# Performance work log

Hardware: AMD Instinct MI355X
Metric: run time of the kernel (lower is better)

The kernel has to match this reference:

```python
import jax, jax.numpy as jnp
import numpy as np

B, N, C, H = 8, 1024, 768, 12
WBITS, ABITS, PGABITS = 8, 8, 4
TH = 0.99  # greater-than mask threshold on MSB softmax


def quant(x, bits):
    """Fixed-point quantize to `bits` bits, straight-through estimator."""
    step = 2.0 ** (1 - bits)
    q = jnp.round(x / step) * step
    return x + jax.lax.stop_gradient(q - x)


def setup_inputs() -> dict:
    key = jax.random.key(0)
    k1, k2, k3 = jax.random.split(key, 3)
    x = jax.random.normal(k1, (B, N, C), jnp.float32)
    # qkv: QLinear(dim, 3*dim, bias=False); proj: QLinear(dim, dim, bias=True)
    w_qkv = jax.random.normal(k2, (3 * C, C), jnp.float32) * (C ** -0.5)
    w_proj = jax.random.normal(k3, (C, C), jnp.float32) * (C ** -0.5)
    b_proj = jnp.zeros((C,), jnp.float32)
    return {"x": x, "w_qkv": w_qkv, "w_proj": w_proj, "b_proj": b_proj}


def reference(x, w_qkv, w_proj, b_proj):
    d = C // H
    scale = d ** -0.5
    # QLinear: quantize activations and weights, then matmul (no qkv bias)
    qkv = quant(x, ABITS) @ quant(w_qkv, WBITS).T            # [B,N,3C]
    qkv = qkv.reshape(B, N, 3, H, d).transpose(2, 0, 3, 1, 4)  # [3,B,H,N,d]
    qkv = quant(qkv, ABITS)
    q, k, v = qkv[0], qkv[1], qkv[2]
    # low-precision MSB pass
    q_msb = quant(q, PGABITS)
    k_msb = quant(k, PGABITS)
    attn_msb = jax.nn.softmax(
        jnp.einsum('bhqd,bhkd->bhqk', q_msb, k_msb) * scale, axis=-1)
    # GreaterThan with straight-through backward (identity grad)
    gt = (attn_msb > TH).astype(attn_msb.dtype)
    mask = attn_msb + jax.lax.stop_gradient(gt - attn_msb)
    # full-precision pass, masked pre-softmax
    attn = jnp.einsum('bhqd,bhkd->bhqk', q, k) * scale * mask
    attn = quant(jax.nn.softmax(attn, axis=-1), ABITS)
    out = jnp.einsum('bhqk,bhkd->bhqd', attn, v)             # [B,H,N,d]
    out = out.transpose(0, 2, 1, 3).reshape(B, N, C)
    return quant(out, ABITS) @ quant(w_proj, WBITS).T + b_proj
```

## Files before the change

### kernel.cpp

```cpp
#include <hip/hip_runtime.h>

#define NB 8
#define NSEQ 1024
#define NC 768
#define NH 12
#define ND 64
#define NM 8192

typedef _Float16 v8h __attribute__((ext_vector_type(8)));
typedef float v4f __attribute__((ext_vector_type(4)));
typedef int   v4i __attribute__((ext_vector_type(4)));

__device__ __forceinline__ float q8f(float x){ return rintf(x*128.f)*0.0078125f; }
__device__ __forceinline__ int imax2(int a, int b){ return a > b ? a : b; }
__device__ __forceinline__ int imin2(int a, int b){ return a < b ? a : b; }

__device__ __forceinline__ int swz(int r, int g){ return (r<<6) + (((g ^ (r & 7)) & 7)<<3); }

__device__ __forceinline__ void async_cp16(const void* g, void* l) {
  __builtin_amdgcn_global_load_lds(
      (const __attribute__((address_space(1))) unsigned int*)g,
      (__attribute__((address_space(3))) unsigned int*)l, 16, 0, 0);
}

__device__ __forceinline__ int idot64(const int* a, const int* b) {
  int si = 0;
#if __has_builtin(__builtin_amdgcn_sdot4)
#pragma unroll
  for (int j = 0; j < 16; j++) si = __builtin_amdgcn_sdot4(a[j], b[j], si, false);
#else
  const char* ca = (const char*)a;
  const char* cb = (const char*)b;
#pragma unroll
  for (int j = 0; j < 64; j++) si += (int)ca[j] * (int)cb[j];
#endif
  return si;
}

__global__ __launch_bounds__(256) void k_pre(const float* __restrict__ x,
                                             const float* __restrict__ wq,
                                             _Float16* __restrict__ xt,
                                             _Float16* __restrict__ wqt) {
  int b = blockIdx.x;
  const float* src; _Float16* dst; int gid;
  if (b < 3072) { src = x;  dst = xt;  gid = b*256 + threadIdx.x; }
  else          { src = wq; dst = wqt; gid = (b-3072)*256 + threadIdx.x; }
  int tile = gid / 12288;
  int rem  = gid - tile*12288;
  int chunk = rem >> 10, idx = rem & 1023;
  int r = idx >> 3, g = idx & 7;
  const float* s = src + (size_t)(tile*128 + r)*768 + chunk*64 + g*8;
  float4 v0 = *(const float4*)s, v1 = *(const float4*)(s + 4);
  v8h o;
  o[0]=(_Float16)q8f(v0.x); o[1]=(_Float16)q8f(v0.y); o[2]=(_Float16)q8f(v0.z); o[3]=(_Float16)q8f(v0.w);
  o[4]=(_Float16)q8f(v1.x); o[5]=(_Float16)q8f(v1.y); o[6]=(_Float16)q8f(v1.z); o[7]=(_Float16)q8f(v1.w);
  *(v8h*)&dst[((size_t)tile*12 + chunk)*8192 + swz(r, g)] = o;
}

__global__ __launch_bounds__(512, 2) void k_qk(const _Float16* __restrict__ xt,
                                               const _Float16* __restrict__ wqt,
                                               const float* __restrict__ bias,
                                               char* __restrict__ QmI,
                                               char* __restrict__ KmI,
                                               float* __restrict__ out) {
  if (blockIdx.x >= 192) {
    int gid = (blockIdx.x - 192)*512 + threadIdx.x;
    int c4 = gid % 192;
    ((float4*)out)[gid] = ((const float4*)bias)[c4];
    return;
  }
  __shared__ _Float16 S[65536];
  _Float16* SA = S;
  _Float16* SB = S + 32768;

  const int tid  = threadIdx.x;
  const int lane = tid & 63;
  const int quad = lane >> 4;
  const int l15  = lane & 15;
  const int wid  = tid >> 6;
  const int wm   = wid >> 2;
  const int wn   = wid & 3;
  const int bx = blockIdx.x & 31, by = blockIdx.x >> 5;
  const int m0 = bx * 256, n0 = by * 256;

  const _Float16* Abase = xt  + (size_t)(2*bx) * 12 * 8192;
  const _Float16* Bbase = wqt + (size_t)(2*by) * 12 * 8192;

  auto stage_half = [&](const _Float16* src, _Float16* dst) {
#pragma unroll
    for (int s = 0; s < 2; s++) {
      int base = (wid*2 + s)*512;
      async_cp16(src + base + lane*8, dst + base);
    }
  };

  v4f acc[8][4] = {};

  stage_half(Abase,               SA);
  stage_half(Abase + 12*8192,     SA + 8192);
  stage_half(Bbase,               SB);
  stage_half(Bbase + 12*8192,     SB + 8192);
  asm volatile("s_waitcnt vmcnt(0)" ::: "memory");
  __builtin_amdgcn_s_barrier();

#pragma unroll 1
  for (int kc = 0; kc < 12; kc++) {
    const int buf = kc & 1;
    const _Float16* A  = &SA[(buf*2 + wm)*8192];
    const _Float16* Bh = &SB[(buf*2 + (wn>>1))*8192];
    _Float16* SAn = &SA[(buf^1)*16384];
    _Float16* SBn = &SB[(buf^1)*16384];

    if (kc + 1 < 12) {
      stage_half(Abase + (size_t)(kc+1)*8192,        SAn);
      stage_half(Abase + (size_t)(12 + kc+1)*8192,   SAn + 8192);
    }

    v8h bf[4][2];
#pragma unroll
    for (int nt = 0; nt < 4; nt++)
#pragma unroll
      for (int ks = 0; ks < 2; ks++)
        bf[nt][ks] = *(const v8h*)&Bh[swz((wn&1)*64 + nt*16 + l15, ks*4 + quad)];

#pragma unroll
    for (int p = 0; p < 4; p++) {
      v8h a[2][2];
#pragma unroll
      for (int mt = 0; mt < 2; mt++)
#pragma unroll
        for (int ks = 0; ks < 2; ks++)
          a[mt][ks] = *(const v8h*)&A[swz((p*2 + mt)*16 + l15, ks*4 + quad)];
      __builtin_amdgcn_s_setprio(1);
#pragma unroll
      for (int ks = 0; ks < 2; ks++)
#pragma unroll
        for (int nt = 0; nt < 4; nt++) {
          acc[p*2+0][nt] = __builtin_amdgcn_mfma_f32_16x16x32_f16(a[0][ks], bf[nt][ks], acc[p*2+0][nt], 0, 0, 0);
          acc[p*2+1][nt] = __builtin_amdgcn_mfma_f32_16x16x32_f16(a[1][ks], bf[nt][ks], acc[p*2+1][nt], 0, 0, 0);
        }
      __builtin_amdgcn_s_setprio(0);
      if (p == 0 && kc + 1 < 12) {
        stage_half(Bbase + (size_t)(kc+1)*8192,        SBn);
        stage_half(Bbase + (size_t)(12 + kc+1)*8192,   SBn + 8192);
      }
    }
    asm volatile("s_waitcnt vmcnt(0)" ::: "memory");
    __builtin_amdgcn_s_barrier();
  }

  char* P8 = (char*)S;
#pragma unroll
  for (int fr = 0; fr < 8; fr++)
#pragma unroll
    for (int nt = 0; nt < 4; nt++)
#pragma unroll
      for (int rr = 0; rr < 4; rr++) {
        float v = q8f(acc[fr][nt][rr]);
        int qi = (int)rintf(v * 8.f);
        int rl = wm*128 + fr*16 + quad*4 + rr;
        int cl = wn*64 + nt*16 + l15;
        P8[rl*272 + cl] = (char)qi;
      }
  __syncthreads();
  const int which = (by >= 3);
  int c0 = n0 - which*768;
#pragma unroll
  for (int t = 0; t < 8; t++) {
    int idx = tid + t*512;
    int r = idx >> 4, cg = idx & 15;
    v4i val = *(const v4i*)&P8[r*272 + cg*16];
    if (!which) {
      *(v4i*)&QmI[(size_t)(m0 + r)*768 + c0 + cg*16] = val;
    } else {
      int m = m0 + r, n = m & 1023, bI = m >> 10;
      int col = c0 + cg*16;
      int h = col >> 6, d0 = col & 63;
      *(v4i*)&KmI[(((size_t)(bI*NH + h)*1024 + n) << 6) + d0] = val;
    }
  }
}

__global__ __launch_bounds__(256) void k_attn(const char* __restrict__ QmI,
                                              const char* __restrict__ KmI,
                                              const float* __restrict__ x,
                                              const float* __restrict__ wqkv,
                                              const float* __restrict__ wproj,
                                              float* __restrict__ out) {
  __shared__ char  S2[2][16384];
  __shared__ float rowm[128];
  __shared__ int   cand[128];
  __shared__ int   hrowA[128];
  __shared__ int   hcolA[128];
  __shared__ float qf[64], kf[64], vf[64];
  __shared__ float od[64];
  __shared__ float pps;
  __shared__ int   cnt, hcnt;

  const int tid  = threadIdx.x;
  const int lane = tid & 63;
  const int quad = lane >> 4;
  const int l15  = lane & 15;
  const int wid  = tid >> 6;
  const int R0   = wid * 16;
  const int bh = blockIdx.x;
  const int q0 = blockIdx.y * 128;
  const int bb = bh / NH, hb = bh % NH;
  const size_t mrow = (size_t)bb * NSEQ;
  const int hoff = hb * 64;
  const char* KmB = KmI + (size_t)bh * 1024 * 64;

  if (tid == 0) { cnt = 0; hcnt = 0; }

  auto stageK = [&](int kp, int bi) {
#pragma unroll
    for (int s = 0; s < 4; s++) {
      int seg = wid*4 + s;
      async_cp16(KmB + kp*16384 + seg*1024 + lane*16, &S2[bi][seg*1024]);
    }
  };

  v4i aQ[2];
#pragma unroll
  for (int b2 = 0; b2 < 2; b2++)
    aQ[b2] = *(const v4i*)&QmI[(mrow + q0 + b2*64 + R0 + l15)*768 + hoff + quad*16];

  int lm[2][4], lm2[2][4];
#pragma unroll
  for (int b2 = 0; b2 < 2; b2++)
#pragma unroll
    for (int r = 0; r < 4; r++) { lm[b2][r] = -1073741824; lm2[b2][r] = -1073741824; }

  stageK(0, 0);
#pragma unroll 1
  for (int kp = 0; kp < 4; kp++) {
    if (kp + 1 < 4) {
      stageK(kp + 1, (kp + 1) & 1);
      asm volatile("s_waitcnt vmcnt(4)" ::: "memory");
    } else {
      asm volatile("s_waitcnt vmcnt(0)" ::: "memory");
    }
    __builtin_amdgcn_s_barrier();
#pragma unroll
    for (int g64 = 0; g64 < 4; g64++) {
      const char* Ks = &S2[kp & 1][g64*4096];
      v4i c0a[4] = {}, c1a[4] = {};
      __builtin_amdgcn_s_setprio(1);
#pragma unroll
      for (int nt = 0; nt < 4; nt++) {
        v4i b = *(const v4i*)&Ks[(nt*16 + l15)*64 + quad*16];
        c0a[nt] = __builtin_amdgcn_mfma_i32_16x16x64_i8(aQ[0], b, c0a[nt], 0, 0, 0);
        c1a[nt] = __builtin_amdgcn_mfma_i32_16x16x64_i8(aQ[1], b, c1a[nt], 0, 0, 0);
      }
      __builtin_amdgcn_s_setprio(0);
#pragma unroll
      for (int r = 0; r < 4; r++) {
        int g0 = imax2(imax2(c0a[0][r], c0a[1][r]), imax2(c0a[2][r], c0a[3][r]));
        lm2[0][r] = imax2(lm2[0][r], imin2(lm[0][r], g0));
        lm[0][r]  = imax2(lm[0][r], g0);
        int g1 = imax2(imax2(c1a[0][r], c1a[1][r]), imax2(c1a[2][r], c1a[3][r]));
        lm2[1][r] = imax2(lm2[1][r], imin2(lm[1][r], g1));
        lm[1][r]  = imax2(lm[1][r], g1);
      }
    }
    __builtin_amdgcn_s_barrier();
  }
#pragma unroll
  for (int b2 = 0; b2 < 2; b2++)
#pragma unroll
    for (int r = 0; r < 4; r++) {
      int m = lm[b2][r], m2 = lm2[b2][r];
#pragma unroll
      for (int o = 1; o < 16; o <<= 1) {
        int om  = __shfl_xor(m, o);
        int om2 = __shfl_xor(m2, o);
        m2 = imax2(imax2(m2, om2), imin2(m, om));
        m  = imax2(m, om);
      }
      if (l15 == 0 && (m - m2) > 2304) {
        int row = b2*64 + R0 + quad*4 + r;
        rowm[row] = (float)m * 0.001953125f;
        int ix = atomicAdd(&cnt, 1);
        cand[ix] = row;
      }
    }
  __syncthreads();

  int nc = cnt;
  for (int ci = wid; ci < nc; ci += 4) {
    int row = cand[ci];
    float m = rowm[row];
    const int* qrow = (const int*)&QmI[(mrow + q0 + row)*768 + hoff];
    int qw[16];
#pragma unroll
    for (int j = 0; j < 16; j++) qw[j] = qrow[j];
    float l = 0.f, bmax = -1e30f;
    int bcol = 0;
    for (int t = 0; t < 16; t++) {
      const int* kb = (const int*)&KmB[(size_t)(t*64 + lane)*64];
      int si = idot64(qw, kb);
      float s = (float)si * 0.001953125f;
      l += expf(s - m);
      if (s > bmax) { bmax = s; bcol = t*64 + lane; }
    }
#pragma unroll
    for (int o = 1; o < 64; o <<= 1) {
      l += __shfl_xor(l, o);
      float ov = __shfl_xor(bmax, o);
      int   oc = __shfl_xor(bcol, o);
      if (ov > bmax || (ov == bmax && oc < bcol)) { bmax = ov; bcol = oc; }
    }
    if (lane == 0 && (1.0f / l) > 0.99f) {
      int ix = atomicAdd(&hcnt, 1);
      hrowA[ix] = row; hcolA[ix] = bcol;
    }
  }
  __syncthreads();

  int nh = hcnt;
  for (int hi = 0; hi < nh; hi++) {
    int row = hrowA[hi], cst = hcolA[hi];
    if (tid < 192) {
      int d = tid & 63, part = tid >> 6;
      int wrow = part*768 + hoff + d;
      int xrow = (part == 0) ? (int)(mrow + q0 + row) : (int)(mrow + cst);
      const float* xr = &x[(size_t)xrow*768];
      const float* wr = &wqkv[(size_t)wrow*768];
      float s = 0.f;
      for (int k = 0; k < 768; k++) s += q8f(xr[k]) * q8f(wr[k]);
      float v = q8f(s);
      if (part == 0) qf[d] = v; else if (part == 1) kf[d] = v; else vf[d] = v;
    }
    __syncthreads();
    if (tid == 0) {
      float s = 0.f;
      for (int d = 0; d < 64; d++) s += qf[d]*kf[d];
      float sf = s * 0.125f;
      float m2 = fmaxf(sf, 0.f);
      float l2 = expf(sf - m2) + 1023.f*expf(-m2);
      pps = rintf(expf(sf - m2)/l2*128.f)*0.0078125f;
    }
    __syncthreads();
    float p = pps;
    if (p != 0.f) {
      if (tid < 64) od[tid] = q8f(p * vf[tid]);
      __syncthreads();
      for (int c = tid; c < 768; c += 256) {
        const float* wr = &wproj[(size_t)c*768 + hoff];
        float s = 0.f;
        for (int d = 0; d < 64; d++) s += od[d] * q8f(wr[d]);
        atomicAdd(&out[(mrow + q0 + row)*768 + c], s);
      }
    }
    __syncthreads();
  }
}

extern "C" void kernel_launch(void* const* d_in, const int* in_sizes, int n_in,
                              void* d_out, int out_size, void* d_ws, size_t ws_size,
                              hipStream_t stream) {
  const float* x      = (const float*)d_in[0];
  const float* w_qkv  = (const float*)d_in[1];
  const float* w_proj = (const float*)d_in[2];
  const float* b_proj = (const float*)d_in[3];
  float* out = (float*)d_out;

  char* p = (char*)d_ws;
  _Float16* xt  = (_Float16*)p;  p += (size_t)NM*768*2;
  _Float16* wqt = (_Float16*)p;  p += (size_t)1536*768*2;
  char* QmI = p;  p += (size_t)NM*768;
  char* KmI = p;  p += (size_t)NM*768;

  k_pre <<<dim3(3648), dim3(256), 0, stream>>>(x, w_qkv, xt, wqt);
  k_qk  <<<dim3(192 + 3072), dim3(512), 0, stream>>>(xt, wqt, b_proj, QmI, KmI, out);
  k_attn<<<dim3(96, 8), dim3(256), 0, stream>>>(QmI, KmI, x, w_qkv, w_proj, out);
}
```

Before: 121.4 us.

## Keep full K tile resident in swizzled LDS and reuse it for candidate rows

```diff
diff --git a/kernel.cpp b/kernel.cpp
--- a/kernel.cpp
+++ b/kernel.cpp
@@ -187,7 +187,7 @@
                                               const float* __restrict__ wqkv,
                                               const float* __restrict__ wproj,
                                               float* __restrict__ out) {
-  __shared__ char  S2[2][16384];
+  __shared__ char  S2[65536];
   __shared__ float rowm[128];
   __shared__ int   cand[128];
   __shared__ int   hrowA[128];
@@ -212,11 +212,14 @@
 
   if (tid == 0) { cnt = 0; hcnt = 0; }
 
-  auto stageK = [&](int kp, int bi) {
+  const int rl  = lane >> 2;
+  const int gsw = (lane & 3) ^ (rl & 3);
+  auto stageK = [&](int kp) {
 #pragma unroll
     for (int s = 0; s < 4; s++) {
       int seg = wid*4 + s;
-      async_cp16(KmB + kp*16384 + seg*1024 + lane*16, &S2[bi][seg*1024]);
+      async_cp16(KmB + kp*16384 + (seg*16 + rl)*64 + (gsw<<4),
+                 &S2[kp*16384 + seg*1024]);
     }
   };
 
@@ -224,6 +227,7 @@
 #pragma unroll
   for (int b2 = 0; b2 < 2; b2++)
     aQ[b2] = *(const v4i*)&QmI[(mrow + q0 + b2*64 + R0 + l15)*768 + hoff + quad*16];
+  asm volatile("s_waitcnt vmcnt(0)" ::: "memory");
 
   int lm[2][4], lm2[2][4];
 #pragma unroll
@@ -231,24 +235,22 @@
 #pragma unroll
     for (int r = 0; r < 4; r++) { lm[b2][r] = -1073741824; lm2[b2][r] = -1073741824; }
 
-  stageK(0, 0);
+  stageK(0);
+  stageK(1);
 #pragma unroll 1
   for (int kp = 0; kp < 4; kp++) {
-    if (kp + 1 < 4) {
-      stageK(kp + 1, (kp + 1) & 1);
-      asm volatile("s_waitcnt vmcnt(4)" ::: "memory");
-    } else {
-      asm volatile("s_waitcnt vmcnt(0)" ::: "memory");
-    }
+    if (kp < 3) asm volatile("s_waitcnt vmcnt(4)" ::: "memory");
+    else        asm volatile("s_waitcnt vmcnt(0)" ::: "memory");
     __builtin_amdgcn_s_barrier();
+    if (kp + 2 < 4) stageK(kp + 2);
 #pragma unroll
     for (int g64 = 0; g64 < 4; g64++) {
-      const char* Ks = &S2[kp & 1][g64*4096];
+      const char* Ks = &S2[kp*16384 + g64*4096];
       v4i c0a[4] = {}, c1a[4] = {};
       __builtin_amdgcn_s_setprio(1);
 #pragma unroll
       for (int nt = 0; nt < 4; nt++) {
-        v4i b = *(const v4i*)&Ks[(nt*16 + l15)*64 + quad*16];
+        v4i b = *(const v4i*)&Ks[(nt*16 + l15)*64 + ((quad ^ (l15 & 3))<<4)];
         c0a[nt] = __builtin_amdgcn_mfma_i32_16x16x64_i8(aQ[0], b, c0a[nt], 0, 0, 0);
         c1a[nt] = __builtin_amdgcn_mfma_i32_16x16x64_i8(aQ[1], b, c1a[nt], 0, 0, 0);
       }
@@ -263,7 +265,6 @@
         lm[1][r]  = imax2(lm[1][r], g1);
       }
     }
-    __builtin_amdgcn_s_barrier();
   }
 #pragma unroll
   for (int b2 = 0; b2 < 2; b2++)
@@ -287,6 +288,7 @@
   __syncthreads();
 
   int nc = cnt;
+  const int xr = lane & 3;
   for (int ci = wid; ci < nc; ci += 4) {
     int row = cand[ci];
     float m = rowm[row];
@@ -297,11 +299,19 @@
     float l = 0.f, bmax = -1e30f;
     int bcol = 0;
     for (int t = 0; t < 16; t++) {
-      const int* kb = (const int*)&KmB[(size_t)(t*64 + lane)*64];
-      int si = idot64(qw, kb);
+      int rk = t*64 + lane;
+      const char* kbase = &S2[rk*64];
+      int kw[16];
+#pragma unroll
+      for (int g4 = 0; g4 < 4; g4++) {
+        v4i kv = *(const v4i*)&kbase[((g4 ^ xr)<<4)];
+        kw[g4*4+0] = kv[0]; kw[g4*4+1] = kv[1];
+        kw[g4*4+2] = kv[2]; kw[g4*4+3] = kv[3];
+      }
+      int si = idot64(qw, kw);
       float s = (float)si * 0.001953125f;
       l += expf(s - m);
-      if (s > bmax) { bmax = s; bcol = t*64 + lane; }
+      if (s > bmax) { bmax = s; bcol = rk; }
     }
 #pragma unroll
     for (int o = 1; o < 64; o <<= 1) {
@@ -324,10 +334,10 @@
       int d = tid & 63, part = tid >> 6;
       int wrow = part*768 + hoff + d;
       int xrow = (part == 0) ? (int)(mrow + q0 + row) : (int)(mrow + cst);
-      const float* xr = &x[(size_t)xrow*768];
+      const float* xr2 = &x[(size_t)xrow*768];
       const float* wr = &wqkv[(size_t)wrow*768];
       float s = 0.f;
-      for (int k = 0; k < 768; k++) s += q8f(xr[k]) * q8f(wr[k]);
+      for (int k = 0; k < 768; k++) s += q8f(xr2[k]) * q8f(wr[k]);
       float v = q8f(s);
       if (part == 0) qf[d] = v; else if (part == 1) kf[d] = v; else vf[d] = v;
     }
```

Result: slower. 132.3 us (+9.0%).

## Fuse input quantization into QK GEMM, removing the pre-pass kernel

Applied to the files above, without the earlier changes.

```diff
diff --git a/kernel.cpp b/kernel.cpp
--- a/kernel.cpp
+++ b/kernel.cpp
@@ -17,48 +17,28 @@
 
 __device__ __forceinline__ int swz(int r, int g){ return (r<<6) + (((g ^ (r & 7)) & 7)<<3); }
 
+__device__ __forceinline__ int idot64(const int* a, const int* b) {
+  int si = 0;
+#if __has_builtin(__builtin_amdgcn_sdot4)
+#pragma unroll
+  for (int j = 0; j < 16; j++) si = __builtin_amdgcn_sdot4(a[j], b[j], si, false);
+#else
+  const char* ca = (const char*)a;
+  const char* cb = (const char*)b;
+#pragma unroll
+  for (int j = 0; j < 64; j++) si += (int)ca[j] * (int)cb[j];
+#endif
+  return si;
+}
+
 __device__ __forceinline__ void async_cp16(const void* g, void* l) {
   __builtin_amdgcn_global_load_lds(
       (const __attribute__((address_space(1))) unsigned int*)g,
       (__attribute__((address_space(3))) unsigned int*)l, 16, 0, 0);
 }
 
-__device__ __forceinline__ int idot64(const int* a, const int* b) {
-  int si = 0;
-#if __has_builtin(__builtin_amdgcn_sdot4)
-#pragma unroll
-  for (int j = 0; j < 16; j++) si = __builtin_amdgcn_sdot4(a[j], b[j], si, false);
-#else
-  const char* ca = (const char*)a;
-  const char* cb = (const char*)b;
-#pragma unroll
-  for (int j = 0; j < 64; j++) si += (int)ca[j] * (int)cb[j];
-#endif
-  return si;
-}
-
-__global__ __launch_bounds__(256) void k_pre(const float* __restrict__ x,
-                                             const float* __restrict__ wq,
-                                             _Float16* __restrict__ xt,
-                                             _Float16* __restrict__ wqt) {
-  int b = blockIdx.x;
-  const float* src; _Float16* dst; int gid;
-  if (b < 3072) { src = x;  dst = xt;  gid = b*256 + threadIdx.x; }
-  else          { src = wq; dst = wqt; gid = (b-3072)*256 + threadIdx.x; }
-  int tile = gid / 12288;
-  int rem  = gid - tile*12288;
-  int chunk = rem >> 10, idx = rem & 1023;
-  int r = idx >> 3, g = idx & 7;
-  const float* s = src + (size_t)(tile*128 + r)*768 + chunk*64 + g*8;
-  float4 v0 = *(const float4*)s, v1 = *(const float4*)(s + 4);
-  v8h o;
-  o[0]=(_Float16)q8f(v0.x); o[1]=(_Float16)q8f(v0.y); o[2]=(_Float16)q8f(v0.z); o[3]=(_Float16)q8f(v0.w);
-  o[4]=(_Float16)q8f(v1.x); o[5]=(_Float16)q8f(v1.y); o[6]=(_Float16)q8f(v1.z); o[7]=(_Float16)q8f(v1.w);
-  *(v8h*)&dst[((size_t)tile*12 + chunk)*8192 + swz(r, g)] = o;
-}
-
-__global__ __launch_bounds__(512, 2) void k_qk(const _Float16* __restrict__ xt,
-                                               const _Float16* __restrict__ wqt,
+__global__ __launch_bounds__(512, 2) void k_qk(const float* __restrict__ x,
+                                               const float* __restrict__ wqkv,
                                                const float* __restrict__ bias,
                                                char* __restrict__ QmI,
                                                char* __restrict__ KmI,
@@ -83,25 +63,35 @@
   const int bx = blockIdx.x & 31, by = blockIdx.x >> 5;
   const int m0 = bx * 256, n0 = by * 256;
 
-  const _Float16* Abase = xt  + (size_t)(2*bx) * 12 * 8192;
-  const _Float16* Bbase = wqt + (size_t)(2*by) * 12 * 8192;
-
-  auto stage_half = [&](const _Float16* src, _Float16* dst) {
-#pragma unroll
-    for (int s = 0; s < 2; s++) {
-      int base = (wid*2 + s)*512;
-      async_cp16(src + base + lane*8, dst + base);
-    }
+  const int h   = tid >> 8;
+  const int t2  = tid & 255;
+  const int rr_ = t2 >> 1;
+  const int gp  = (t2 & 1) * 4;
+
+  auto ldq = [&](const float* src, int row0, int kc, int g0, float4* f) {
+    const float* sp = src + (size_t)(row0 + h*128 + rr_)*768 + kc*64 + g0*8;
+    f[0] = ((const float4*)sp)[0]; f[1] = ((const float4*)sp)[1];
+    f[2] = ((const float4*)sp)[2]; f[3] = ((const float4*)sp)[3];
   };
+  auto wrq = [&](_Float16* dstbuf, int g0, const float4* f) {
+#pragma unroll
+    for (int gi = 0; gi < 2; gi++) {
+      const float* ff = (const float*)&f[gi*2];
+      v8h o;
+#pragma unroll
+      for (int j = 0; j < 8; j++) o[j] = (_Float16)q8f(ff[j]);
+      *(v8h*)&dstbuf[h*8192 + swz(rr_, g0 + gi)] = o;
+    }
+  };
 
   v4f acc[8][4] = {};
-
-  stage_half(Abase,               SA);
-  stage_half(Abase + 12*8192,     SA + 8192);
-  stage_half(Bbase,               SB);
-  stage_half(Bbase + 12*8192,     SB + 8192);
-  asm volatile("s_waitcnt vmcnt(0)" ::: "memory");
-  __builtin_amdgcn_s_barrier();
+  float4 fa[4], fb[4];
+
+  ldq(x,    m0, 0, gp,     fa);  wrq(SA, gp,     fa);
+  ldq(x,    m0, 0, gp + 2, fa);  wrq(SA, gp + 2, fa);
+  ldq(wqkv, n0, 0, gp,     fb);  wrq(SB, gp,     fb);
+  ldq(wqkv, n0, 0, gp + 2, fb);  wrq(SB, gp + 2, fb);
+  __syncthreads();
 
 #pragma unroll 1
   for (int kc = 0; kc < 12; kc++) {
@@ -110,11 +100,9 @@
     const _Float16* Bh = &SB[(buf*2 + (wn>>1))*8192];
     _Float16* SAn = &SA[(buf^1)*16384];
     _Float16* SBn = &SB[(buf^1)*16384];
-
-    if (kc + 1 < 12) {
-      stage_half(Abase + (size_t)(kc+1)*8192,        SAn);
-      stage_half(Abase + (size_t)(12 + kc+1)*8192,   SAn + 8192);
-    }
+    const bool pre = (kc + 1 < 12);
+
+    if (pre) ldq(x, m0, kc + 1, gp, fa);
 
     v8h bf[4][2];
 #pragma unroll
@@ -140,13 +128,14 @@
           acc[p*2+1][nt] = __builtin_amdgcn_mfma_f32_16x16x32_f16(a[1][ks], bf[nt][ks], acc[p*2+1][nt], 0, 0, 0);
         }
       __builtin_amdgcn_s_setprio(0);
-      if (p == 0 && kc + 1 < 12) {
-        stage_half(Bbase + (size_t)(kc+1)*8192,        SBn);
-        stage_half(Bbase + (size_t)(12 + kc+1)*8192,   SBn + 8192);
-      }
-    }
-    asm volatile("s_waitcnt vmcnt(0)" ::: "memory");
-    __builtin_amdgcn_s_barrier();
+      if (pre) {
+        if (p == 0) { wrq(SAn, gp,     fa); ldq(x,    m0, kc + 1, gp + 2, fa); }
+        if (p == 1) { wrq(SAn, gp + 2, fa); ldq(wqkv, n0, kc + 1, gp,     fb); }
+        if (p == 2) { wrq(SBn, gp,     fb); ldq(wqkv, n0, kc + 1, gp + 2, fb); }
+        if (p == 3) { wrq(SBn, gp + 2, fb); }
+      }
+    }
+    __syncthreads();
   }
 
   char* P8 = (char*)S;
@@ -175,8 +164,8 @@
     } else {
       int m = m0 + r, n = m & 1023, bI = m >> 10;
       int col = c0 + cg*16;
-      int h = col >> 6, d0 = col & 63;
-      *(v4i*)&KmI[(((size_t)(bI*NH + h)*1024 + n) << 6) + d0] = val;
+      int hh = col >> 6, d0 = col & 63;
+      *(v4i*)&KmI[(((size_t)(bI*NH + hh)*1024 + n) << 6) + d0] = val;
     }
   }
 }
@@ -324,10 +313,10 @@
       int d = tid & 63, part = tid >> 6;
       int wrow = part*768 + hoff + d;
       int xrow = (part == 0) ? (int)(mrow + q0 + row) : (int)(mrow + cst);
-      const float* xr = &x[(size_t)xrow*768];
+      const float* xr2 = &x[(size_t)xrow*768];
       const float* wr = &wqkv[(size_t)wrow*768];
       float s = 0.f;
-      for (int k = 0; k < 768; k++) s += q8f(xr[k]) * q8f(wr[k]);
+      for (int k = 0; k < 768; k++) s += q8f(xr2[k]) * q8f(wr[k]);
       float v = q8f(s);
       if (part == 0) qf[d] = v; else if (part == 1) kf[d] = v; else vf[d] = v;
     }
@@ -366,12 +355,9 @@
   float* out = (float*)d_out;
 
   char* p = (char*)d_ws;
-  _Float16* xt  = (_Float16*)p;  p += (size_t)NM*768*2;
-  _Float16* wqt = (_Float16*)p;  p += (size_t)1536*768*2;
   char* QmI = p;  p += (size_t)NM*768;
   char* KmI = p;  p += (size_t)NM*768;
 
-  k_pre <<<dim3(3648), dim3(256), 0, stream>>>(x, w_qkv, xt, wqt);
-  k_qk  <<<dim3(192 + 3072), dim3(512), 0, stream>>>(xt, wqt, b_proj, QmI, KmI, out);
+  k_qk  <<<dim3(192 + 3072), dim3(512), 0, stream>>>(x, w_qkv, b_proj, QmI, KmI, out);
   k_attn<<<dim3(96, 8), dim3(256), 0, stream>>>(QmI, KmI, x, w_qkv, w_proj, out);
 }
```

After: 148.9 us. 22.7% more time.
